# Kernel tuning notes

Hardware: AMD Instinct MI355X
Metric: run time of the kernel (lower is better)

Reference implementation:

```python
import jax, jax.numpy as jnp
import numpy as np

B, N, D, H, FF = 4, 1024, 512, 8, 2048
DH = D // H
RPE_HID = 16
COORD_DIM = 2


def _ln(x, g, b, eps=1e-5):
    m = jnp.mean(x, axis=-1, keepdims=True)
    v = jnp.mean((x - m) ** 2, axis=-1, keepdims=True)
    return (x - m) * jax.lax.rsqrt(v + eps) * g + b


def setup_inputs() -> dict:
    key = jax.random.key(0)
    ks = jax.random.split(key, 20)
    s = 0.02
    inp = {
        "x": jax.random.normal(ks[0], (B, N, D), dtype=jnp.float32),
        "coords": jax.random.uniform(ks[1], (B, N, COORD_DIM), dtype=jnp.float32),
        # qkv + output projections
        "Wq": jax.random.normal(ks[2], (D, D), jnp.float32) * s,
        "bq": jnp.zeros((D,), jnp.float32),
        "Wk": jax.random.normal(ks[3], (D, D), jnp.float32) * s,
        "bk": jnp.zeros((D,), jnp.float32),
        "Wv": jax.random.normal(ks[4], (D, D), jnp.float32) * s,
        "bv": jnp.zeros((D,), jnp.float32),
        "Wo": jax.random.normal(ks[5], (D, D), jnp.float32) * s,
        "bo": jnp.zeros((D,), jnp.float32),
        # learned per-head logit scale (Swin-v2 style cosine attention)
        "logit_scale": jnp.full((H, 1, 1), np.log(10.0), jnp.float32),
        # absolute positional embedder PE: Linear(2 -> D)
        "W_pe": jax.random.normal(ks[6], (COORD_DIM, D), jnp.float32) * s,
        "b_pe": jnp.zeros((D,), jnp.float32),
        # relative positional embedder RPE: MLP(2 -> 16 -> H)
        "W_r1": jax.random.normal(ks[7], (COORD_DIM, RPE_HID), jnp.float32) * 0.5,
        "b_r1": jnp.zeros((RPE_HID,), jnp.float32),
        "W_r2": jax.random.normal(ks[8], (RPE_HID, H), jnp.float32) * 0.5,
        "b_r2": jnp.zeros((H,), jnp.float32),
        # layernorm params
        "g_peq": jnp.ones((D,), jnp.float32), "bt_peq": jnp.zeros((D,), jnp.float32),
        "g_pek": jnp.ones((D,), jnp.float32), "bt_pek": jnp.zeros((D,), jnp.float32),
        "g2": jnp.ones((D,), jnp.float32), "bt2": jnp.zeros((D,), jnp.float32),
        "g3": jnp.ones((D,), jnp.float32), "bt3": jnp.zeros((D,), jnp.float32),
        # MLP (bias=False)
        "W_ff1": jax.random.normal(ks[9], (D, FF), jnp.float32) * s,
        "W_ff2": jax.random.normal(ks[10], (FF, D), jnp.float32) * s,
    }
    return inp


def reference(x, coords, Wq, bq, Wk, bk, Wv, bv, Wo, bo, logit_scale,
              W_pe, b_pe, W_r1, b_r1, W_r2, b_r2,
              g_peq, bt_peq, g_pek, bt_pek, g2, bt2, g3, bt3,
              W_ff1, W_ff2):
    # --- PE add + LayerNorm on q and k (self-attention: coords_cross_ = coords)
    pe = coords @ W_pe + b_pe                      # [B,N,D]
    q = _ln(x + pe, g_peq, bt_peq)
    k = _ln(x + pe, g_pek, bt_pek)
    v = x                                          # v is NOT PE-normed in source

    # --- relative-position bias from cartesian coord differences
    rel = coords[:, :, None, :] - coords[:, None, :, :]   # [B,Nq,Nk,2]
    hid = jax.nn.relu(rel @ W_r1 + b_r1)                  # [B,Nq,Nk,16]
    bias = hid @ W_r2 + b_r2                              # [B,Nq,Nk,H]
    bias = jnp.transpose(bias, (0, 3, 1, 2))              # [B,H,Nq,Nk]

    # --- multi-head cosine attention with learned logit scale
    qp = (q @ Wq + bq).reshape(B, N, H, DH)
    kp = (k @ Wk + bk).reshape(B, N, H, DH)
    vp = (v @ Wv + bv).reshape(B, N, H, DH)
    qn = qp / jnp.maximum(jnp.linalg.norm(qp, axis=-1, keepdims=True), 1e-12)
    kn = kp / jnp.maximum(jnp.linalg.norm(kp, axis=-1, keepdims=True), 1e-12)
    scale = jnp.exp(jnp.minimum(logit_scale, jnp.log(100.0)))  # [H,1,1]
    attn = jnp.einsum('bqhd,bkhd->bhqk', qn, kn) * scale[None] + bias
    attn = jax.nn.softmax(attn, axis=-1)
    att_out = jnp.einsum('bhqk,bkhd->bqhd', attn, vp).reshape(B, N, D)
    att_out = att_out @ Wo + bo

    # --- residual + norm + MLP (LeakyReLU 0.2 after each linear) + residual + norm
    x1 = _ln(x + att_out, g2, bt2)
    mlp = jax.nn.leaky_relu(
        jax.nn.leaky_relu(x1 @ W_ff1, 0.2) @ W_ff2, 0.2)
    return _ln(x1 + mlp, g3, bt3)
```

## Files before the change

kernel.cpp:

```cpp
#include <hip/hip_runtime.h>

#define BB 4
#define NN 1024
#define DD 512
#define HH 8
#define DHH 64
#define FFF 2048

typedef __attribute__((ext_vector_type(8))) short bf16x8;
typedef __attribute__((ext_vector_type(4))) float f32x4;

__device__ inline float wave_sum(float v) {
#pragma unroll
  for (int off = 32; off; off >>= 1) v += __shfl_xor(v, off);
  return v;
}

__device__ inline unsigned short cvt_bf16(float f) {
  union { float f; unsigned u; } x;
  x.f = f;
  unsigned r = x.u + 0x7FFFu + ((x.u >> 16) & 1u);
  return (unsigned short)(r >> 16);
}

__device__ __forceinline__ void gl_lds16(const void* g, void* l) {
  __builtin_amdgcn_global_load_lds(
      (__attribute__((address_space(1))) void*)(g),
      (__attribute__((address_space(3))) void*)(l), 16, 0, 0);
}

__global__ __launch_bounds__(256) void wconv_kernel(
    const float* __restrict__ W0, const float* __restrict__ W1,
    const float* __restrict__ W2, const float* __restrict__ W3,
    const float* __restrict__ W4, const float* __restrict__ W5,
    unsigned short* __restrict__ out) {
  int bidx = blockIdx.x;
  const float* W; unsigned short* Wt; int K, N, local;
  if (bidx < 256) {
    int sel = bidx >> 6; local = bidx & 63;
    W = sel == 0 ? W0 : sel == 1 ? W1 : sel == 2 ? W2 : W3;
    K = 512; N = 512; Wt = out + (size_t)sel * 262144;
  } else if (bidx < 512) {
    local = bidx - 256; W = W4; K = 512; N = 2048; Wt = out + 1048576;
  } else {
    local = bidx - 512; W = W5; K = 2048; N = 512; Wt = out + 2097152;
  }
  int ntn = N >> 6;
  int tn = (local & (ntn - 1)) << 6, tk = (local / ntn) << 6;
  __shared__ float tile[64][65];
  int tid = threadIdx.x;
#pragma unroll
  for (int i = 0; i < 16; ++i) {
    int e = tid + i * 256, kk = e >> 6, nn = e & 63;
    tile[kk][nn] = W[(size_t)(tk + kk) * N + tn + nn];
  }
  __syncthreads();
#pragma unroll
  for (int i = 0; i < 16; ++i) {
    int e = tid + i * 256, nn = e >> 6, kk = e & 63;
    Wt[(size_t)(tn + nn) * K + tk + kk] = cvt_bf16(tile[kk][nn]);
  }
}

__global__ __launch_bounds__(256) void bias_kernel(
    const float* __restrict__ coords,
    const float* __restrict__ W_r1, const float* __restrict__ b_r1,
    const float* __restrict__ W_r2, const float* __restrict__ b_r2,
    unsigned short* __restrict__ bias_out) {
  int kt = blockIdx.x, qt = blockIdx.y, b = blockIdx.z;
  int tid = threadIdx.x;
  int q = qt * 64 + (tid >> 2);
  int k0 = kt * 32 + (tid & 3) * 8;
  float cq0 = coords[((size_t)b * NN + q) * 2 + 0];
  float cq1 = coords[((size_t)b * NN + q) * 2 + 1];
  float Aq[16];
#pragma unroll
  for (int l = 0; l < 16; ++l)
    Aq[l] = fmaf(cq0, W_r1[l], fmaf(cq1, W_r1[16 + l], b_r1[l]));
  float ck0[8], ck1[8];
#pragma unroll
  for (int kk = 0; kk < 8; ++kk) {
    ck0[kk] = coords[((size_t)b * NN + k0 + kk) * 2 + 0];
    ck1[kk] = coords[((size_t)b * NN + k0 + kk) * 2 + 1];
  }
  float acc[8][8];
#pragma unroll
  for (int kk = 0; kk < 8; ++kk)
#pragma unroll
    for (int h = 0; h < 8; ++h) acc[kk][h] = b_r2[h];
#pragma unroll
  for (int l = 0; l < 16; ++l) {
    float w1a = W_r1[l], w1b = W_r1[16 + l];
#pragma unroll
    for (int kk = 0; kk < 8; ++kk) {
      float hv = Aq[l] - fmaf(ck0[kk], w1a, ck1[kk] * w1b);
      hv = fmaxf(hv, 0.f);
#pragma unroll
      for (int h = 0; h < 8; ++h)
        acc[kk][h] = fmaf(hv, W_r2[l * HH + h], acc[kk][h]);
    }
  }
#pragma unroll
  for (int h = 0; h < 8; ++h) {
    bf16x8 ov;
#pragma unroll
    for (int kk = 0; kk < 8; ++kk) ov[kk] = (short)cvt_bf16(acc[kk][h]);
    *(bf16x8*)&bias_out[(((size_t)b * HH + h) * NN + q) * NN + k0] = ov;
  }
}

__global__ __launch_bounds__(512) void pe_ln_kernel(
    const float* __restrict__ x, const float* __restrict__ coords,
    const float* __restrict__ W_pe, const float* __restrict__ b_pe,
    const float* __restrict__ g_q, const float* __restrict__ bt_q,
    const float* __restrict__ g_k, const float* __restrict__ bt_k,
    unsigned short* __restrict__ q_lnb, unsigned short* __restrict__ k_lnb,
    unsigned short* __restrict__ x_bf) {
  int row = blockIdx.x;
  int tid = threadIdx.x;
  float c0 = coords[(size_t)row * 2 + 0];
  float c1 = coords[(size_t)row * 2 + 1];
  size_t idx = (size_t)row * DD + tid;
  float xv = x[idx];
  x_bf[idx] = cvt_bf16(xv);
  float val = xv + c0 * W_pe[tid] + c1 * W_pe[DD + tid] + b_pe[tid];

  __shared__ float ws[8], ws2[8];
  float s = wave_sum(val);
  if ((tid & 63) == 0) ws[tid >> 6] = s;
  __syncthreads();
  float mean = 0.f;
#pragma unroll
  for (int w = 0; w < 8; ++w) mean += ws[w];
  mean *= (1.f / DD);
  float dv = val - mean;
  float s2 = wave_sum(dv * dv);
  if ((tid & 63) == 0) ws2[tid >> 6] = s2;
  __syncthreads();
  float var = 0.f;
#pragma unroll
  for (int w = 0; w < 8; ++w) var += ws2[w];
  var *= (1.f / DD);
  float rstd = rsqrtf(var + 1e-5f);
  q_lnb[idx] = cvt_bf16(dv * rstd * g_q[tid] + bt_q[tid]);
  k_lnb[idx] = cvt_bf16(dv * rstd * g_k[tid] + bt_k[tid]);
}

__global__ __launch_bounds__(512) void add_ln_kernel(
    const float* __restrict__ a, const float* __restrict__ r,
    const float* __restrict__ g, const float* __restrict__ bt,
    float* __restrict__ out, unsigned short* __restrict__ out_bf) {
  int row = blockIdx.x;
  int tid = threadIdx.x;
  size_t idx = (size_t)row * DD + tid;
  float val = a[idx] + r[idx];
  __shared__ float ws[8], ws2[8];
  float s = wave_sum(val);
  if ((tid & 63) == 0) ws[tid >> 6] = s;
  __syncthreads();
  float mean = 0.f;
#pragma unroll
  for (int w = 0; w < 8; ++w) mean += ws[w];
  mean *= (1.f / DD);
  float dv = val - mean;
  float s2 = wave_sum(dv * dv);
  if ((tid & 63) == 0) ws2[tid >> 6] = s2;
  __syncthreads();
  float var = 0.f;
#pragma unroll
  for (int w = 0; w < 8; ++w) var += ws2[w];
  var *= (1.f / DD);
  float rstd = rsqrtf(var + 1e-5f);
  float o = dv * rstd * g[tid] + bt[tid];
  out[idx] = o;
  if (out_bf) out_bf[idx] = cvt_bf16(o);
}

template <int ACT, int EPI>
__global__ __launch_bounds__(256) void mgemm_kernel(
    const unsigned short* __restrict__ A, const unsigned short* __restrict__ BT,
    const float* __restrict__ bias, void* __restrict__ C,
    int M, int Nc, int K) {
  __shared__ unsigned short lds[4][8192];
  int tid = threadIdx.x;
  int w = tid >> 6, lane = tid & 63, lg = lane >> 4, lr = lane & 15;
  int bm = blockIdx.y * 128, bn = blockIdx.x * 128;
  int wr = w >> 1, wc = w & 1;

  int segl = lane >> 3;
  int cb = (lane & 7) << 4;

  f32x4 zf = {0.f, 0.f, 0.f, 0.f};
  f32x4 acc[4][4];
#pragma unroll
  for (int mi = 0; mi < 4; ++mi)
#pragma unroll
    for (int ni = 0; ni < 4; ++ni) acc[mi][ni] = zf;

  int nt = K >> 6;

  auto STAGE = [&](int buf, int t) {
    int k0 = t << 6;
#pragma unroll
    for (int i = 0; i < 4; ++i) {
      int seg = w * 4 + i;
      int r = (seg << 3) + segl;
      int csw = cb ^ ((r & 7) << 4);
      const char* ga = (const char*)A + (((size_t)(bm + r) * K + k0) << 1) + csw;
      gl_lds16(ga, &lds[buf * 2][seg << 9]);
      const char* gb = (const char*)BT + (((size_t)(bn + r) * K + k0) << 1) + csw;
      gl_lds16(gb, &lds[buf * 2 + 1][seg << 9]);
    }
  };

  auto COMPUTE = [&](int buf) {
    const unsigned short* As = lds[buf * 2];
    const unsigned short* Bs = lds[buf * 2 + 1];
    bf16x8 af[2][4], bfr[2][4];
#pragma unroll
    for (int kh = 0; kh < 2; ++kh)
#pragma unroll
      for (int mi = 0; mi < 4; ++mi) {
        int r = wr * 64 + mi * 16 + lr;
        int e = (r << 6) + (kh << 5) + (lg << 3);
        af[kh][mi] = *(const bf16x8*)&As[e ^ ((r & 7) << 3)];
        int rb = wc * 64 + mi * 16 + lr;
        int eb = (rb << 6) + (kh << 5) + (lg << 3);
        bfr[kh][mi] = *(const bf16x8*)&Bs[eb ^ ((rb & 7) << 3)];
      }
#pragma unroll
    for (int kh = 0; kh < 2; ++kh)
#pragma unroll
      for (int mi = 0; mi < 4; ++mi)
#pragma unroll
        for (int ni = 0; ni < 4; ++ni)
          acc[mi][ni] = __builtin_amdgcn_mfma_f32_16x16x32_bf16(
              af[kh][mi], bfr[kh][ni], acc[mi][ni], 0, 0, 0);
  };

  STAGE(0, 0);
  __syncthreads();
  for (int t = 0; t < nt; ++t) {
    if (t + 1 < nt) STAGE((t + 1) & 1, t + 1);
    COMPUTE(t & 1);
    __syncthreads();
  }

  if (EPI <= 1) {
#pragma unroll
    for (int ni = 0; ni < 4; ++ni) {
      int col = bn + wc * 64 + ni * 16 + lr;
      float bv = bias ? bias[col] : 0.f;
#pragma unroll
      for (int mi = 0; mi < 4; ++mi) {
#pragma unroll
        for (int j = 0; j < 4; ++j) {
          int row = bm + wr * 64 + mi * 16 + lg * 4 + j;
          float v = acc[mi][ni][j] + bv;
          if (ACT == 1) v = v > 0.f ? v : 0.2f * v;
          if (EPI == 1)
            ((unsigned short*)C)[(size_t)row * Nc + col] = cvt_bf16(v);
          else
            ((float*)C)[(size_t)row * Nc + col] = v;
        }
      }
    }
  } else {
    int h = (bn >> 6) + wc;
    float bvf[4];
#pragma unroll
    for (int ni = 0; ni < 4; ++ni) bvf[ni] = bias[bn + wc * 64 + ni * 16 + lr];
#pragma unroll
    for (int mi = 0; mi < 4; ++mi) {
#pragma unroll
      for (int j = 0; j < 4; ++j) {
        float vals[4]; float ss = 0.f;
#pragma unroll
        for (int ni = 0; ni < 4; ++ni) {
          float v = acc[mi][ni][j] + bvf[ni];
          vals[ni] = v;
          ss = fmaf(v, v, ss);
        }
        float rn = 1.f;
        if (EPI == 2) {
          ss += __shfl_xor(ss, 1);
          ss += __shfl_xor(ss, 2);
          ss += __shfl_xor(ss, 4);
          ss += __shfl_xor(ss, 8);
          rn = 1.f / fmaxf(sqrtf(ss), 1e-12f);
        }
        int row = bm + wr * 64 + mi * 16 + lg * 4 + j;
        int b_ = row >> 10, n_ = row & (NN - 1);
        unsigned short* ob =
            (unsigned short*)C + (((size_t)b_ * HH + h) * NN + n_) * DHH;
#pragma unroll
        for (int ni = 0; ni < 4; ++ni)
          ob[ni * 16 + lr] = cvt_bf16(vals[ni] * rn);
      }
    }
  }
}

template <int NSPLIT>
__global__ __launch_bounds__(256) void attn_mfma_kernel(
    const unsigned short* __restrict__ qb, const unsigned short* __restrict__ kb,
    const unsigned short* __restrict__ vb,
    const unsigned short* __restrict__ bias_g,
    const float* __restrict__ logit_scale,
    unsigned short* __restrict__ attb,
    unsigned short* __restrict__ part, int nb) {
  int qt = blockIdx.x, h = blockIdx.y;
  int b = blockIdx.z % nb, sp = blockIdx.z / nb;
  int tid = threadIdx.x;
  int w = tid >> 6, lane = tid & 63;
  int lg = lane >> 4, lr = lane & 15;

  __shared__ unsigned short vt[2][4096];
  __shared__ unsigned short bt[2][4096];
  __shared__ unsigned short pl[4][1024];

  const size_t bh = ((size_t)b * HH + h) * NN;
  const int NT = (NN / 64) / NSPLIT;
  const int kt0 = sp * NT;

  int q_glob = qt * 64 + w * 16 + lr;
  bf16x8 aq0 = *(const bf16x8*)&qb[(bh + q_glob) * DHH + lg * 8];
  bf16x8 aq1 = *(const bf16x8*)&qb[(bh + q_glob) * DHH + 32 + lg * 8];

  float scale_h = __expf(fminf(logit_scale[h], 4.605170185988091f));

  float m_run[4] = {-1e30f, -1e30f, -1e30f, -1e30f};
  float l_run[4] = {0.f, 0.f, 0.f, 0.f};
  f32x4 zf = {0.f, 0.f, 0.f, 0.f};
  f32x4 acc_o[4] = {zf, zf, zf, zf};

  auto STAGE = [&](int buf, int t) {
    int ktg = kt0 + t;
#pragma unroll
    for (int it = 0; it < 2; ++it) {
      int kl = it * 32 + (tid & 31);
      int d0 = (tid >> 5) * 8;
      bf16x8 vv = *(const bf16x8*)&vb[(bh + ktg * 64 + kl) * DHH + d0];
#pragma unroll
      for (int j = 0; j < 8; ++j) {
        int d = d0 + j;
        vt[buf][(d * 64 + kl) ^ ((d & 7) << 3)] = (unsigned short)vv[j];
      }
    }
#pragma unroll
    for (int c = 0; c < 2; ++c) {
      int seg = w * 2 + c;
      int ql = seg * 8 + (lane >> 3);
      int ks = ((lane & 7) * 8) ^ (((ql >> 2) & 3) << 4);
      const unsigned short* src =
          &bias_g[(bh + qt * 64 + ql) * NN + ktg * 64 + ks];
      gl_lds16(src, &bt[buf][seg * 512]);
    }
  };

  STAGE(0, 0);
  __syncthreads();

  for (int t = 0; t < NT; ++t) {
    int cur = t & 1;
    if (t + 1 < NT) STAGE(cur ^ 1, t + 1);
    int ktg = kt0 + t;

    f32x4 s_acc[4];
#pragma unroll
    for (int kc = 0; kc < 4; ++kc) {
      const unsigned short* krow =
          &kb[(bh + ktg * 64 + kc * 16 + lr) * DHH + lg * 8];
      bf16x8 bk0 = *(const bf16x8*)krow;
      bf16x8 bk1 = *(const bf16x8*)(krow + 32);
      s_acc[kc] = __builtin_amdgcn_mfma_f32_16x16x32_bf16(aq0, bk0, zf, 0, 0, 0);
      s_acc[kc] = __builtin_amdgcn_mfma_f32_16x16x32_bf16(aq1, bk1, s_acc[kc], 0, 0, 0);
    }

#pragma unroll
    for (int kc = 0; kc < 4; ++kc)
#pragma unroll
      for (int r = 0; r < 4; ++r) {
        int qrow = w * 16 + lg * 4 + r;
        unsigned short ub =
            bt[cur][qrow * 64 + ((kc * 16 + lr) ^ (lg << 4))];
        float bf_ = __uint_as_float(((unsigned)ub) << 16);
        s_acc[kc][r] = fmaf(s_acc[kc][r], scale_h, bf_);
      }

    float pf[4][4];
#pragma unroll
    for (int r = 0; r < 4; ++r) {
      float mx = fmaxf(fmaxf(s_acc[0][r], s_acc[1][r]),
                       fmaxf(s_acc[2][r], s_acc[3][r]));
      mx = fmaxf(mx, __shfl_xor(mx, 1));
      mx = fmaxf(mx, __shfl_xor(mx, 2));
      mx = fmaxf(mx, __shfl_xor(mx, 4));
      mx = fmaxf(mx, __shfl_xor(mx, 8));
      float m_new = fmaxf(m_run[r], mx);
      float alpha = __expf(m_run[r] - m_new);
      m_run[r] = m_new;
      float ps = 0.f;
#pragma unroll
      for (int kc = 0; kc < 4; ++kc) {
        float p = __expf(s_acc[kc][r] - m_new);
        pf[kc][r] = p;
        ps += p;
      }
      l_run[r] = l_run[r] * alpha + ps;
#pragma unroll
      for (int ds = 0; ds < 4; ++ds) acc_o[ds][r] *= alpha;
    }

#pragma unroll
    for (int kc = 0; kc < 4; ++kc)
#pragma unroll
      for (int r = 0; r < 4; ++r) {
        int q = lg * 4 + r;
        pl[w][(q * 64 + kc * 16 + lr) ^ ((q & 7) << 3)] = cvt_bf16(pf[kc][r]);
      }

#pragma unroll
    for (int ka = 0; ka < 2; ++ka) {
      bf16x8 pa = *(const bf16x8*)&pl[w][(lr * 64 + ka * 32 + lg * 8) ^
                                         ((lr & 7) << 3)];
#pragma unroll
      for (int ds = 0; ds < 4; ++ds) {
        int d = ds * 16 + lr;
        bf16x8 bv =
            *(const bf16x8*)&vt[cur][(d * 64 + ka * 32 + lg * 8) ^ ((d & 7) << 3)];
        acc_o[ds] = __builtin_amdgcn_mfma_f32_16x16x32_bf16(pa, bv, acc_o[ds], 0, 0, 0);
      }
    }
    __syncthreads();
  }

#pragma unroll
  for (int r = 0; r < 4; ++r) {
    l_run[r] += __shfl_xor(l_run[r], 1);
    l_run[r] += __shfl_xor(l_run[r], 2);
    l_run[r] += __shfl_xor(l_run[r], 4);
    l_run[r] += __shfl_xor(l_run[r], 8);
  }

  if (NSPLIT == 1) {
#pragma unroll
    for (int ds = 0; ds < 4; ++ds)
#pragma unroll
      for (int r = 0; r < 4; ++r) {
        int qg = qt * 64 + w * 16 + lg * 4 + r;
        attb[((size_t)b * NN + qg) * DD + h * DHH + ds * 16 + lr] =
            cvt_bf16(acc_o[ds][r] / l_run[r]);
      }
  } else {
#pragma unroll
    for (int r = 0; r < 4; ++r) {
      int qg = qt * 64 + w * 16 + lg * 4 + r;
      size_t idx = ((size_t)(sp * nb + b) * HH + h) * NN + qg;
      unsigned short* pr = part + idx * 68;
#pragma unroll
      for (int ds = 0; ds < 4; ++ds)
        pr[ds * 16 + lr] = cvt_bf16(acc_o[ds][r]);
      if (lr == 0) {
        *(float*)(pr + 64) = m_run[r];
        *(float*)(pr + 66) = l_run[r];
      }
    }
  }
}

__global__ __launch_bounds__(256) void combine_kernel(
    const unsigned short* __restrict__ part, unsigned short* __restrict__ attb,
    int nb) {
  int tid = threadIdx.x;
  int w = tid >> 6, d = tid & 63;
  int row = blockIdx.x * 4 + w;
  int b = row >> 13, rem = row & 8191, h = rem >> 10, n = rem & (NN - 1);
  size_t i0 = ((size_t)b * HH + h) * NN + n;
  size_t i1 = i0 + (size_t)nb * HH * NN;
  const unsigned short* p0 = part + i0 * 68;
  const unsigned short* p1 = part + i1 * 68;
  float m0 = *(const float*)(p0 + 64), l0 = *(const float*)(p0 + 66);
  float m1 = *(const float*)(p1 + 64), l1 = *(const float*)(p1 + 66);
  float ms = fmaxf(m0, m1);
  float w0 = __expf(m0 - ms), w1 = __expf(m1 - ms);
  float a0 = __uint_as_float(((unsigned)p0[d]) << 16);
  float a1 = __uint_as_float(((unsigned)p1[d]) << 16);
  float o = (a0 * w0 + a1 * w1) / (l0 * w0 + l1 * w1);
  attb[((size_t)b * NN + n) * DD + h * DHH + d] = cvt_bf16(o);
}

extern "C" void kernel_launch(void* const* d_in, const int* in_sizes, int n_in,
                              void* d_out, int out_size, void* d_ws, size_t ws_size,
                              hipStream_t stream) {
  const float* x      = (const float*)d_in[0];
  const float* coords = (const float*)d_in[1];
  const float* Wq = (const float*)d_in[2];  const float* bq = (const float*)d_in[3];
  const float* Wk = (const float*)d_in[4];  const float* bk = (const float*)d_in[5];
  const float* Wv = (const float*)d_in[6];  const float* bv = (const float*)d_in[7];
  const float* Wo = (const float*)d_in[8];  const float* bo = (const float*)d_in[9];
  const float* logit_scale = (const float*)d_in[10];
  const float* W_pe = (const float*)d_in[11]; const float* b_pe = (const float*)d_in[12];
  const float* W_r1 = (const float*)d_in[13]; const float* b_r1 = (const float*)d_in[14];
  const float* W_r2 = (const float*)d_in[15]; const float* b_r2 = (const float*)d_in[16];
  const float* g_peq = (const float*)d_in[17]; const float* bt_peq = (const float*)d_in[18];
  const float* g_pek = (const float*)d_in[19]; const float* bt_pek = (const float*)d_in[20];
  const float* g2 = (const float*)d_in[21]; const float* bt2 = (const float*)d_in[22];
  const float* g3 = (const float*)d_in[23]; const float* bt3 = (const float*)d_in[24];
  const float* W_ff1 = (const float*)d_in[25];
  const float* W_ff2 = (const float*)d_in[26];
  float* out = (float*)d_out;

  const size_t T = (size_t)BB * NN;
  char* wsb = (char*)d_ws;
  const size_t U = 4u * 1024u * 1024u;

  unsigned short* wt_all = (unsigned short*)(wsb + 0 * U);
  unsigned short* WqT   = wt_all;
  unsigned short* WkT   = wt_all + 262144;
  unsigned short* WvT   = wt_all + 524288;
  unsigned short* WoT   = wt_all + 786432;
  unsigned short* Wff1T = wt_all + 1048576;
  unsigned short* Wff2T = wt_all + 2097152;
  unsigned short* q_lnb = (unsigned short*)(wsb + 2 * U);
  unsigned short* k_lnb = (unsigned short*)(wsb + 3 * U);
  unsigned short* x_bf  = (unsigned short*)(wsb + 4 * U);
  unsigned short* q_bf  = (unsigned short*)(wsb + 5 * U);
  unsigned short* k_bf  = (unsigned short*)(wsb + 6 * U);
  unsigned short* v_bf  = (unsigned short*)(wsb + 7 * U);
  unsigned short* att_bf = (unsigned short*)(wsb + 8 * U);
  float* proj = (float*)(wsb + 9 * U);
  float* x1   = (float*)(wsb + 11 * U);
  unsigned short* x1_bf = (unsigned short*)(wsb + 13 * U);
  unsigned short* hid_bf = (unsigned short*)(wsb + 2 * U);
  float* mlp  = (float*)(wsb + 9 * U);
  unsigned short* part_ws = (unsigned short*)(wsb + 2 * U);
  unsigned short* bias_ws = (unsigned short*)(wsb + 9 * U);

  const int full_path = (ws_size >= 25 * U) ? 1 : 0;

  wconv_kernel<<<dim3(768), dim3(256), 0, stream>>>(
      Wq, Wk, Wv, Wo, W_ff1, W_ff2, wt_all);

  pe_ln_kernel<<<dim3(T), dim3(512), 0, stream>>>(
      x, coords, W_pe, b_pe, g_peq, bt_peq, g_pek, bt_pek, q_lnb, k_lnb, x_bf);

  mgemm_kernel<0, 2><<<dim3(DD / 128, T / 128), dim3(256), 0, stream>>>(
      q_lnb, WqT, bq, q_bf, (int)T, DD, DD);
  mgemm_kernel<0, 2><<<dim3(DD / 128, T / 128), dim3(256), 0, stream>>>(
      k_lnb, WkT, bk, k_bf, (int)T, DD, DD);
  mgemm_kernel<0, 3><<<dim3(DD / 128, T / 128), dim3(256), 0, stream>>>(
      x_bf, WvT, bv, v_bf, (int)T, DD, DD);

  if (full_path) {
    bias_kernel<<<dim3(NN / 32, NN / 64, BB), dim3(256), 0, stream>>>(
        coords, W_r1, b_r1, W_r2, b_r2, bias_ws);
    attn_mfma_kernel<2><<<dim3(NN / 64, HH, 2 * BB), dim3(256), 0, stream>>>(
        q_bf, k_bf, v_bf, bias_ws, logit_scale, nullptr, part_ws, BB);
    combine_kernel<<<dim3(BB * HH * NN / 4), dim3(256), 0, stream>>>(
        part_ws, att_bf, BB);
  } else {
    for (int b = 0; b < BB; ++b) {
      bias_kernel<<<dim3(NN / 32, NN / 64, 1), dim3(256), 0, stream>>>(
          coords + (size_t)b * NN * 2, W_r1, b_r1, W_r2, b_r2, bias_ws);
      attn_mfma_kernel<1><<<dim3(NN / 64, HH, 1), dim3(256), 0, stream>>>(
          q_bf + (size_t)b * HH * NN * DHH, k_bf + (size_t)b * HH * NN * DHH,
          v_bf + (size_t)b * HH * NN * DHH, bias_ws, logit_scale,
          att_bf + (size_t)b * NN * DD, nullptr, 1);
    }
  }

  mgemm_kernel<0, 0><<<dim3(DD / 128, T / 128), dim3(256), 0, stream>>>(
      att_bf, WoT, bo, proj, (int)T, DD, DD);

  add_ln_kernel<<<dim3(T), dim3(512), 0, stream>>>(x, proj, g2, bt2, x1, x1_bf);

  mgemm_kernel<1, 1><<<dim3(FFF / 128, T / 128), dim3(256), 0, stream>>>(
      x1_bf, Wff1T, nullptr, hid_bf, (int)T, FFF, DD);
  mgemm_kernel<1, 0><<<dim3(DD / 128, T / 128), dim3(256), 0, stream>>>(
      hid_bf, Wff2T, nullptr, mlp, (int)T, DD, FFF);

  add_ln_kernel<<<dim3(T), dim3(512), 0, stream>>>(x1, mlp, g3, bt3, out, nullptr);
}
```

Measured before the change: 202.4 us.

## Fuse QKV GEMMs into one launch, pre-transpose V, drop attention LDS staging

Merges the three Q/K/V projection GEMM launches into one kernel indexed by blockIdx.z. The V projection's epilogue now writes V transposed (head, d, n) to global memory. The attention kernel reads V fragments and bias values straight from global into registers, prefetching the next tile's bias, and drops the LDS transpose staging and per-iteration __syncthreads. This removes launch overhead, the in-kernel V transpose, and block-level barriers. In exchange, V and bias are read from global per wave with no shared-memory reuse across waves, and the transposed V stores are strided and uncoalesced.

```diff
diff --git a/kernel.cpp b/kernel.cpp
--- a/kernel.cpp
+++ b/kernel.cpp
@@ -246,65 +246,143 @@
     __syncthreads();
   }
 
-  if (EPI <= 1) {
-#pragma unroll
-    for (int ni = 0; ni < 4; ++ni) {
-      int col = bn + wc * 64 + ni * 16 + lr;
-      float bv = bias ? bias[col] : 0.f;
+#pragma unroll
+  for (int ni = 0; ni < 4; ++ni) {
+    int col = bn + wc * 64 + ni * 16 + lr;
+    float bv = bias ? bias[col] : 0.f;
+#pragma unroll
+    for (int mi = 0; mi < 4; ++mi) {
+#pragma unroll
+      for (int j = 0; j < 4; ++j) {
+        int row = bm + wr * 64 + mi * 16 + lg * 4 + j;
+        float v = acc[mi][ni][j] + bv;
+        if (ACT == 1) v = v > 0.f ? v : 0.2f * v;
+        if (EPI == 1)
+          ((unsigned short*)C)[(size_t)row * Nc + col] = cvt_bf16(v);
+        else
+          ((float*)C)[(size_t)row * Nc + col] = v;
+      }
+    }
+  }
+}
+
+__global__ __launch_bounds__(256) void qkv_gemm_kernel(
+    const unsigned short* __restrict__ q_lnb,
+    const unsigned short* __restrict__ k_lnb,
+    const unsigned short* __restrict__ x_bf,
+    const unsigned short* __restrict__ wt,
+    const float* __restrict__ bq, const float* __restrict__ bk,
+    const float* __restrict__ bv_,
+    unsigned short* __restrict__ q_bf, unsigned short* __restrict__ k_bf,
+    unsigned short* __restrict__ vt_g) {
+  int z = blockIdx.z;
+  const unsigned short* A = z == 0 ? q_lnb : z == 1 ? k_lnb : x_bf;
+  const unsigned short* BT = wt + (size_t)z * 262144;
+  const float* bias = z == 0 ? bq : z == 1 ? bk : bv_;
+
+  __shared__ unsigned short lds[4][8192];
+  int tid = threadIdx.x;
+  int w = tid >> 6, lane = tid & 63, lg = lane >> 4, lr = lane & 15;
+  int bm = blockIdx.y * 128, bn = blockIdx.x * 128;
+  int wr = w >> 1, wc = w & 1;
+  int segl = lane >> 3;
+  int cb = (lane & 7) << 4;
+
+  f32x4 zf = {0.f, 0.f, 0.f, 0.f};
+  f32x4 acc[4][4];
+#pragma unroll
+  for (int mi = 0; mi < 4; ++mi)
+#pragma unroll
+    for (int ni = 0; ni < 4; ++ni) acc[mi][ni] = zf;
+
+  auto STAGE = [&](int buf, int t) {
+    int k0 = t << 6;
+#pragma unroll
+    for (int i = 0; i < 4; ++i) {
+      int seg = w * 4 + i;
+      int r = (seg << 3) + segl;
+      int csw = cb ^ ((r & 7) << 4);
+      const char* ga = (const char*)A + (((size_t)(bm + r) * DD + k0) << 1) + csw;
+      gl_lds16(ga, &lds[buf * 2][seg << 9]);
+      const char* gb = (const char*)BT + (((size_t)(bn + r) * DD + k0) << 1) + csw;
+      gl_lds16(gb, &lds[buf * 2 + 1][seg << 9]);
+    }
+  };
+  auto COMPUTE = [&](int buf) {
+    const unsigned short* As = lds[buf * 2];
+    const unsigned short* Bs = lds[buf * 2 + 1];
+    bf16x8 af[2][4], bfr[2][4];
+#pragma unroll
+    for (int kh = 0; kh < 2; ++kh)
 #pragma unroll
       for (int mi = 0; mi < 4; ++mi) {
-#pragma unroll
-        for (int j = 0; j < 4; ++j) {
-          int row = bm + wr * 64 + mi * 16 + lg * 4 + j;
-          float v = acc[mi][ni][j] + bv;
-          if (ACT == 1) v = v > 0.f ? v : 0.2f * v;
-          if (EPI == 1)
-            ((unsigned short*)C)[(size_t)row * Nc + col] = cvt_bf16(v);
-          else
-            ((float*)C)[(size_t)row * Nc + col] = v;
-        }
-      }
-    }
-  } else {
-    int h = (bn >> 6) + wc;
-    float bvf[4];
-#pragma unroll
-    for (int ni = 0; ni < 4; ++ni) bvf[ni] = bias[bn + wc * 64 + ni * 16 + lr];
-#pragma unroll
-    for (int mi = 0; mi < 4; ++mi) {
-#pragma unroll
-      for (int j = 0; j < 4; ++j) {
-        float vals[4]; float ss = 0.f;
-#pragma unroll
-        for (int ni = 0; ni < 4; ++ni) {
-          float v = acc[mi][ni][j] + bvf[ni];
-          vals[ni] = v;
-          ss = fmaf(v, v, ss);
-        }
-        float rn = 1.f;
-        if (EPI == 2) {
-          ss += __shfl_xor(ss, 1);
-          ss += __shfl_xor(ss, 2);
-          ss += __shfl_xor(ss, 4);
-          ss += __shfl_xor(ss, 8);
-          rn = 1.f / fmaxf(sqrtf(ss), 1e-12f);
-        }
-        int row = bm + wr * 64 + mi * 16 + lg * 4 + j;
-        int b_ = row >> 10, n_ = row & (NN - 1);
-        unsigned short* ob =
-            (unsigned short*)C + (((size_t)b_ * HH + h) * NN + n_) * DHH;
+        int r = wr * 64 + mi * 16 + lr;
+        int e = (r << 6) + (kh << 5) + (lg << 3);
+        af[kh][mi] = *(const bf16x8*)&As[e ^ ((r & 7) << 3)];
+        int rb = wc * 64 + mi * 16 + lr;
+        int eb = (rb << 6) + (kh << 5) + (lg << 3);
+        bfr[kh][mi] = *(const bf16x8*)&Bs[eb ^ ((rb & 7) << 3)];
+      }
+#pragma unroll
+    for (int kh = 0; kh < 2; ++kh)
+#pragma unroll
+      for (int mi = 0; mi < 4; ++mi)
+#pragma unroll
+        for (int ni = 0; ni < 4; ++ni)
+          acc[mi][ni] = __builtin_amdgcn_mfma_f32_16x16x32_bf16(
+              af[kh][mi], bfr[kh][ni], acc[mi][ni], 0, 0, 0);
+  };
+
+  STAGE(0, 0);
+  __syncthreads();
+  for (int t = 0; t < 8; ++t) {
+    if (t + 1 < 8) STAGE((t + 1) & 1, t + 1);
+    COMPUTE(t & 1);
+    __syncthreads();
+  }
+
+  int h = (bn >> 6) + wc;
+  float bvf[4];
+#pragma unroll
+  for (int ni = 0; ni < 4; ++ni) bvf[ni] = bias[bn + wc * 64 + ni * 16 + lr];
+#pragma unroll
+  for (int mi = 0; mi < 4; ++mi) {
+#pragma unroll
+    for (int j = 0; j < 4; ++j) {
+      float vals[4]; float ss = 0.f;
+#pragma unroll
+      for (int ni = 0; ni < 4; ++ni) {
+        float v = acc[mi][ni][j] + bvf[ni];
+        vals[ni] = v;
+        ss = fmaf(v, v, ss);
+      }
+      int row = bm + wr * 64 + mi * 16 + lg * 4 + j;
+      int b_ = row >> 10, n_ = row & (NN - 1);
+      if (z <= 1) {
+        ss += __shfl_xor(ss, 1);
+        ss += __shfl_xor(ss, 2);
+        ss += __shfl_xor(ss, 4);
+        ss += __shfl_xor(ss, 8);
+        float rn = 1.f / fmaxf(sqrtf(ss), 1e-12f);
+        unsigned short* ob = (z == 0 ? q_bf : k_bf) +
+                             (((size_t)b_ * HH + h) * NN + n_) * DHH;
 #pragma unroll
         for (int ni = 0; ni < 4; ++ni)
           ob[ni * 16 + lr] = cvt_bf16(vals[ni] * rn);
+      } else {
+#pragma unroll
+        for (int ni = 0; ni < 4; ++ni)
+          vt_g[(((size_t)b_ * HH + h) * DHH + ni * 16 + lr) * NN + n_] =
+              cvt_bf16(vals[ni]);
       }
     }
   }
 }
 
 template <int NSPLIT>
-__global__ __launch_bounds__(256) void attn_mfma_kernel(
+__global__ __launch_bounds__(256) void attn_wave_kernel(
     const unsigned short* __restrict__ qb, const unsigned short* __restrict__ kb,
-    const unsigned short* __restrict__ vb,
+    const unsigned short* __restrict__ vtg,
     const unsigned short* __restrict__ bias_g,
     const float* __restrict__ logit_scale,
     unsigned short* __restrict__ attb,
@@ -315,11 +393,10 @@
   int w = tid >> 6, lane = tid & 63;
   int lg = lane >> 4, lr = lane & 15;
 
-  __shared__ unsigned short vt[2][4096];
-  __shared__ unsigned short bt[2][4096];
   __shared__ unsigned short pl[4][1024];
 
   const size_t bh = ((size_t)b * HH + h) * NN;
+  const size_t vbase = ((size_t)b * HH + h) * DHH * NN;
   const int NT = (NN / 64) / NSPLIT;
   const int kt0 = sp * NT;
 
@@ -328,42 +405,25 @@
   bf16x8 aq1 = *(const bf16x8*)&qb[(bh + q_glob) * DHH + 32 + lg * 8];
 
   float scale_h = __expf(fminf(logit_scale[h], 4.605170185988091f));
+
+  const unsigned short* brow[4];
+#pragma unroll
+  for (int r = 0; r < 4; ++r)
+    brow[r] = &bias_g[(bh + qt * 64 + w * 16 + lg * 4 + r) * NN + lr];
 
   float m_run[4] = {-1e30f, -1e30f, -1e30f, -1e30f};
   float l_run[4] = {0.f, 0.f, 0.f, 0.f};
   f32x4 zf = {0.f, 0.f, 0.f, 0.f};
   f32x4 acc_o[4] = {zf, zf, zf, zf};
 
-  auto STAGE = [&](int buf, int t) {
-    int ktg = kt0 + t;
-#pragma unroll
-    for (int it = 0; it < 2; ++it) {
-      int kl = it * 32 + (tid & 31);
-      int d0 = (tid >> 5) * 8;
-      bf16x8 vv = *(const bf16x8*)&vb[(bh + ktg * 64 + kl) * DHH + d0];
-#pragma unroll
-      for (int j = 0; j < 8; ++j) {
-        int d = d0 + j;
-        vt[buf][(d * 64 + kl) ^ ((d & 7) << 3)] = (unsigned short)vv[j];
-      }
-    }
-#pragma unroll
-    for (int c = 0; c < 2; ++c) {
-      int seg = w * 2 + c;
-      int ql = seg * 8 + (lane >> 3);
-      int ks = ((lane & 7) * 8) ^ (((ql >> 2) & 3) << 4);
-      const unsigned short* src =
-          &bias_g[(bh + qt * 64 + ql) * NN + ktg * 64 + ks];
-      gl_lds16(src, &bt[buf][seg * 512]);
-    }
-  };
-
-  STAGE(0, 0);
-  __syncthreads();
-
+  unsigned short bu[4][4];
+#pragma unroll
+  for (int r = 0; r < 4; ++r)
+#pragma unroll
+    for (int kc = 0; kc < 4; ++kc) bu[kc][r] = brow[r][kt0 * 64 + kc * 16];
+
+#pragma unroll 2
   for (int t = 0; t < NT; ++t) {
-    int cur = t & 1;
-    if (t + 1 < NT) STAGE(cur ^ 1, t + 1);
     int ktg = kt0 + t;
 
     f32x4 s_acc[4];
@@ -377,14 +437,20 @@
       s_acc[kc] = __builtin_amdgcn_mfma_f32_16x16x32_bf16(aq1, bk1, s_acc[kc], 0, 0, 0);
     }
 
+    unsigned short bu2[4][4];
+    if (t + 1 < NT) {
+#pragma unroll
+      for (int r = 0; r < 4; ++r)
+#pragma unroll
+        for (int kc = 0; kc < 4; ++kc)
+          bu2[kc][r] = brow[r][(ktg + 1) * 64 + kc * 16];
+    }
+
 #pragma unroll
     for (int kc = 0; kc < 4; ++kc)
 #pragma unroll
       for (int r = 0; r < 4; ++r) {
-        int qrow = w * 16 + lg * 4 + r;
-        unsigned short ub =
-            bt[cur][qrow * 64 + ((kc * 16 + lr) ^ (lg << 4))];
-        float bf_ = __uint_as_float(((unsigned)ub) << 16);
+        float bf_ = __uint_as_float(((unsigned)bu[kc][r]) << 16);
         s_acc[kc][r] = fmaf(s_acc[kc][r], scale_h, bf_);
       }
 
@@ -427,12 +493,18 @@
 #pragma unroll
       for (int ds = 0; ds < 4; ++ds) {
         int d = ds * 16 + lr;
-        bf16x8 bv =
-            *(const bf16x8*)&vt[cur][(d * 64 + ka * 32 + lg * 8) ^ ((d & 7) << 3)];
+        bf16x8 bv = *(const bf16x8*)&vtg[vbase + (size_t)d * NN +
+                                         ktg * 64 + ka * 32 + lg * 8];
         acc_o[ds] = __builtin_amdgcn_mfma_f32_16x16x32_bf16(pa, bv, acc_o[ds], 0, 0, 0);
       }
     }
-    __syncthreads();
+
+    if (t + 1 < NT) {
+#pragma unroll
+      for (int r = 0; r < 4; ++r)
+#pragma unroll
+        for (int kc = 0; kc < 4; ++kc) bu[kc][r] = bu2[kc][r];
+    }
   }
 
 #pragma unroll
@@ -516,9 +588,6 @@
   const size_t U = 4u * 1024u * 1024u;
 
   unsigned short* wt_all = (unsigned short*)(wsb + 0 * U);
-  unsigned short* WqT   = wt_all;
-  unsigned short* WkT   = wt_all + 262144;
-  unsigned short* WvT   = wt_all + 524288;
   unsigned short* WoT   = wt_all + 786432;
   unsigned short* Wff1T = wt_all + 1048576;
   unsigned short* Wff2T = wt_all + 2097152;
@@ -545,17 +614,13 @@
   pe_ln_kernel<<<dim3(T), dim3(512), 0, stream>>>(
       x, coords, W_pe, b_pe, g_peq, bt_peq, g_pek, bt_pek, q_lnb, k_lnb, x_bf);
 
-  mgemm_kernel<0, 2><<<dim3(DD / 128, T / 128), dim3(256), 0, stream>>>(
-      q_lnb, WqT, bq, q_bf, (int)T, DD, DD);
-  mgemm_kernel<0, 2><<<dim3(DD / 128, T / 128), dim3(256), 0, stream>>>(
-      k_lnb, WkT, bk, k_bf, (int)T, DD, DD);
-  mgemm_kernel<0, 3><<<dim3(DD / 128, T / 128), dim3(256), 0, stream>>>(
-      x_bf, WvT, bv, v_bf, (int)T, DD, DD);
+  qkv_gemm_kernel<<<dim3(DD / 128, T / 128, 3), dim3(256), 0, stream>>>(
+      q_lnb, k_lnb, x_bf, wt_all, bq, bk, bv, q_bf, k_bf, v_bf);
 
   if (full_path) {
     bias_kernel<<<dim3(NN / 32, NN / 64, BB), dim3(256), 0, stream>>>(
         coords, W_r1, b_r1, W_r2, b_r2, bias_ws);
-    attn_mfma_kernel<2><<<dim3(NN / 64, HH, 2 * BB), dim3(256), 0, stream>>>(
+    attn_wave_kernel<2><<<dim3(NN / 64, HH, 2 * BB), dim3(256), 0, stream>>>(
         q_bf, k_bf, v_bf, bias_ws, logit_scale, nullptr, part_ws, BB);
     combine_kernel<<<dim3(BB * HH * NN / 4), dim3(256), 0, stream>>>(
         part_ws, att_bf, BB);
@@ -563,9 +628,9 @@
     for (int b = 0; b < BB; ++b) {
       bias_kernel<<<dim3(NN / 32, NN / 64, 1), dim3(256), 0, stream>>>(
           coords + (size_t)b * NN * 2, W_r1, b_r1, W_r2, b_r2, bias_ws);
-      attn_mfma_kernel<1><<<dim3(NN / 64, HH, 1), dim3(256), 0, stream>>>(
+      attn_wave_kernel<1><<<dim3(NN / 64, HH, 1), dim3(256), 0, stream>>>(
           q_bf + (size_t)b * HH * NN * DHH, k_bf + (size_t)b * HH * NN * DHH,
-          v_bf + (size_t)b * HH * NN * DHH, bias_ws, logit_scale,
+          v_bf + (size_t)b * HH * DHH * NN, bias_ws, logit_scale,
           att_bf + (size_t)b * NN * DD, nullptr, 1);
     }
   }
```

Measured after the change: 198.1 us. 1.02x faster.
